# Performance work log

Measured on AMD Instinct MI355X. Metric: run time of the kernel, lower is better.

The kernel has to match this reference:

```python
import jax, jax.numpy as jnp
import numpy as np

B, T, IN_DIM, N_UNITS, OUT_DIM = 512, 64, 21, 128, 1
D = IN_DIM - 2  # 19 features fed to FF_attention_module
NPP_IDX, POPU_IDX = 0, 16
INIT_STD = 0.02


def setup_inputs() -> dict:
    key = jax.random.key(0)
    ks = jax.random.split(key, 21)
    init = lambda k, shape: jax.random.normal(k, shape, jnp.float32) * INIT_STD
    n = N_UNITS
    return {
        "x": jax.random.normal(ks[0], (B, T, IN_DIM), jnp.float32),
        "U_j": init(ks[1], (D, 1, n)),
        "W_j": init(ks[2], (D, n, n)),
        "b_j": init(ks[3], (D, n)),
        "Wi_w": init(ks[4], (D * n, D * (n + 1))),
        "Wi_b": init(ks[5], (D * n,)),
        "Wf_w": init(ks[6], (D * n, D * (n + 1))),
        "Wf_b": init(ks[7], (D * n,)),
        "Wo_w": init(ks[8], (D * n, D * (n + 1))),
        "Wo_b": init(ks[9], (D * n,)),
        "F_alpha_n": init(ks[10], (D, n, 1)),
        "F_alpha_n_b": init(ks[11], (D, 1)),
        "Fbeta_w": init(ks[12], (1, 2 * n)),
        "Fbeta_b": init(ks[13], (1,)),
        "Phi_w": init(ks[14], (OUT_DIM, 2 * n)),
        "Phi_b": init(ks[15], (OUT_DIM,)),
        "fa_w": init(ks[16], (1, 1)),
        "fa_b": init(ks[17], (1,)),
        "hs_w": init(ks[18], (1, 1)),
        "hs_b": init(ks[19], (1,)),
    }


def reference(x, U_j, W_j, b_j, Wi_w, Wi_b, Wf_w, Wf_b, Wo_w, Wo_b,
              F_alpha_n, F_alpha_n_b, Fbeta_w, Fbeta_b, Phi_w, Phi_b,
              fa_w, fa_b, hs_w, hs_b):
    # --- feature slicing for the IMV-LSTM branch (variational dropout is eval-mode identity) ---
    x_FF = jnp.concatenate([x[:, :, :POPU_IDX], x[:, :, -3:]], axis=-1)  # [B,T,D]
    bsz = x.shape[0]

    def step(carry, x_t):
        h, c = carry  # h: [B,D,n], c: [B,D*n]
        # per-variable candidate: tanh(h @ W_j + x_t * U_j + b_j)
        j = jnp.tanh(jnp.einsum('bij,ijk->bik', h, W_j)
                     + x_t[:, :, None] * U_j[:, 0, :]
                     + b_j)  # [B,D,n]
        inp = jnp.concatenate([x_t, h.reshape(bsz, -1)], axis=1)  # [B, D*(n+1)]
        i = jax.nn.sigmoid(inp @ Wi_w.T + Wi_b)
        f = jax.nn.sigmoid(inp @ Wf_w.T + Wf_b)
        o = jax.nn.sigmoid(inp @ Wo_w.T + Wo_b)
        c = c * f + i * j.reshape(bsz, -1)
        h = (o * jnp.tanh(c)).reshape(bsz, D, N_UNITS)
        return (h, c), h

    h0 = jnp.zeros((bsz, D, N_UNITS), x.dtype)
    c0 = jnp.zeros((bsz, D * N_UNITS), x.dtype)
    (h_fin, _), outs = jax.lax.scan(step, (h0, c0), jnp.swapaxes(x_FF, 0, 1))
    outputs = jnp.transpose(outs, (1, 0, 2, 3))  # [B,T,D,n]

    # temporal attention (alphas) over T
    alphas = jnp.exp(jnp.tanh(jnp.einsum('btij,ijk->btik', outputs, F_alpha_n) + F_alpha_n_b))
    alphas = alphas / jnp.sum(alphas, axis=1, keepdims=True)  # [B,T,D,1]
    g_n = jnp.sum(alphas * outputs, axis=1)  # [B,D,n]

    hg = jnp.concatenate([g_n, h_fin], axis=2)  # [B,D,2n]
    mu = hg @ Phi_w.T + Phi_b  # [B,D,OUT_DIM]
    betas = jnp.exp(jnp.tanh(hg @ Fbeta_w.T + Fbeta_b))  # [B,D,1]
    betas = betas / jnp.sum(betas, axis=1, keepdims=True)
    mean = jnp.sum(betas * mu, axis=1)  # [B,OUT_DIM]
    f_FF = jax.nn.sigmoid(mean)

    # limitation gates on last timestep
    f_npp = jax.nn.sigmoid(x[:, -1, NPP_IDX:NPP_IDX + 1] @ fa_w.T + fa_b)
    f_popu = jax.nn.sigmoid(x[:, -1, POPU_IDX:POPU_IDX + 1] @ hs_w.T + hs_b)
    return f_FF * f_npp * f_popu
```

## Files before the change

### kernel.cpp

```cpp
#include <hip/hip_runtime.h>
#include <hip/hip_bf16.h>


#define B_SZ 512
#define T_SZ 64
#define IN_DIMX 21
#define D_F 19
#define G_SZ 2432
#define NPAIR 9728
#define NK16 154
#define HFRAGS 152

typedef __attribute__((ext_vector_type(8))) short bf16x8;
typedef __attribute__((ext_vector_type(16))) float f32x16;

__device__ __forceinline__ float sigmoidf_(float v) { return 1.0f / (1.0f + expf(-v)); }
__device__ __forceinline__ int fmap(int j) { return j < 16 ? j : j + 2; }

__device__ __forceinline__ size_t hidx(int b, int gg) {
    int mb2 = b >> 6, r = b & 63, mi = r >> 5, bl = r & 31;
    int k16 = gg >> 4, half = (gg >> 3) & 1, e = gg & 7;
    return ((((size_t)(mb2 * 2 + mi) * HFRAGS + k16) * 64) + bl + 32 * half) * 8 + e;
}

__global__ __launch_bounds__(256) void prep_kernel(
    const float* __restrict__ x,
    const float* __restrict__ Wi, const float* __restrict__ Wf, const float* __restrict__ Wo,
    const float* __restrict__ Wj,
    __hip_bfloat16* __restrict__ Wt2,
    __hip_bfloat16* __restrict__ Wjt2,
    __hip_bfloat16* __restrict__ xfr,
    __hip_bfloat16* __restrict__ hfr0,
    float* __restrict__ apre)
{
    int i = blockIdx.x * 256 + threadIdx.x;
    const int NWT = 3 * 19 * 4 * NK16 * 512;
    if (i < NWT) {
        int e = i & 7, lane = (i >> 3) & 63, fi = i >> 9;
        int k16 = fi % NK16, ff = fi / NK16;
        int s = ff & 3, ff2 = ff >> 2;
        int d = ff2 % 19, gate = ff2 / 19;
        int gcol = d * 128 + s * 32 + (lane & 31);
        int k = k16 * 16 + (lane >> 5) * 8 + e;
        const float* W = gate == 0 ? Wi : (gate == 1 ? Wf : Wo);
        float v = 0.0f;
        if (k < 2432)      v = W[gcol * 2451 + 19 + k];
        else if (k < 2451) v = W[gcol * 2451 + (k - 2432)];
        Wt2[i] = __float2bfloat16(v);
        return;
    }
    i -= NWT;
    if (i < 19 * 4 * 8 * 512) {
        int e = i & 7, lane = (i >> 3) & 63, fi = i >> 9;
        int k16 = fi & 7, ff = fi >> 3;
        int s = ff & 3, d = ff >> 2;
        int col = s * 32 + (lane & 31);
        int kin = k16 * 16 + (lane >> 5) * 8 + e;
        Wjt2[i] = __float2bfloat16(Wj[d * 16384 + kin * 128 + col]);
        return;
    }
    i -= 19 * 4 * 8 * 512;
    if (i < 64 * 8 * 2 * 2 * 512) {
        int e = i & 7, lane = (i >> 3) & 63, fi = i >> 9;
        int k16 = fi & 1, ff = fi >> 1;
        int mi = ff & 1, ff2 = ff >> 1;
        int mb = ff2 & 7, tt = ff2 >> 3;
        int b = mb * 64 + mi * 32 + (lane & 31);
        int kloc = k16 * 16 + (lane >> 5) * 8 + e;
        float v = 0.0f;
        if (kloc < 19) v = x[(b * T_SZ + tt) * IN_DIMX + fmap(kloc)];
        xfr[i] = __float2bfloat16(v);
        return;
    }
    i -= 64 * 8 * 2 * 2 * 512;
    if (i < 8 * 2 * HFRAGS * 512) { hfr0[i] = __float2bfloat16(0.0f); return; }
    i -= 8 * 2 * HFRAGS * 512;
    if (i < 2 * NPAIR) apre[i] = 0.0f;
}

#define LOADSET(aa0, aa1, b00, b01, b10, b11, b20, b21, kk) do { \
    int f_ = 2 * (kk); \
    if ((kk) == 76) { aa0 = pAx[0]; aa1 = pAx[64]; } \
    else { aa0 = pA[(size_t)f_ * 64]; aa1 = pA[(size_t)f_ * 64 + 64]; } \
    b00 = pB0[(size_t)f_ * 64]; b01 = pB0[(size_t)f_ * 64 + 64]; \
    b10 = pB1[(size_t)f_ * 64]; b11 = pB1[(size_t)f_ * 64 + 64]; \
    b20 = pB2[(size_t)f_ * 64]; b21 = pB2[(size_t)f_ * 64 + 64]; } while (0)

#define MFMASET(aa0, aa1, b00, b01, b10, b11, b20, b21) do { \
    acc0 = __builtin_amdgcn_mfma_f32_32x32x16_bf16(aa0, b00, acc0, 0, 0, 0); \
    acc1 = __builtin_amdgcn_mfma_f32_32x32x16_bf16(aa0, b10, acc1, 0, 0, 0); \
    acc2 = __builtin_amdgcn_mfma_f32_32x32x16_bf16(aa0, b20, acc2, 0, 0, 0); \
    acc0 = __builtin_amdgcn_mfma_f32_32x32x16_bf16(aa1, b01, acc0, 0, 0, 0); \
    acc1 = __builtin_amdgcn_mfma_f32_32x32x16_bf16(aa1, b11, acc1, 0, 0, 0); \
    acc2 = __builtin_amdgcn_mfma_f32_32x32x16_bf16(aa1, b21, acc2, 0, 0, 0); } while (0)

__global__ __launch_bounds__(512, 2) void step_kernel(
    int t,
    const __hip_bfloat16* __restrict__ Wt2,
    const __hip_bfloat16* __restrict__ Wjt2,
    const __hip_bfloat16* __restrict__ xfr,
    const __hip_bfloat16* __restrict__ hcur,
    __hip_bfloat16* __restrict__ hnext,
    float* __restrict__ cbuf,
    float* __restrict__ apre,
    float* __restrict__ asum,
    float* __restrict__ gacc,
    const float* __restrict__ x,
    const float* __restrict__ Uj, const float* __restrict__ bj,
    const float* __restrict__ Wib, const float* __restrict__ Wfb, const float* __restrict__ Wob,
    const float* __restrict__ Fa, const float* __restrict__ Fab)
{
    __shared__ __align__(16) __hip_bfloat16 strans[8][1024];
    const int tid = threadIdx.x;
    const int g = 19 * (blockIdx.x & 7) + (blockIdx.x >> 3);
    const int nb = g >> 3, mb = g & 7;
    const int w = tid >> 6, lane = tid & 63;
    const int mi = w >> 2, s = w & 3;

    const bf16x8* pA  = (const bf16x8*)hcur + ((size_t)(mb * 2 + mi) * HFRAGS) * 64 + lane;
    const bf16x8* pAx = (const bf16x8*)xfr + ((size_t)((t * 8 + mb) * 2 + mi) * 2) * 64 + lane;
    const bf16x8* pB0 = (const bf16x8*)Wt2 + ((size_t)(0 * 76 + nb * 4 + s) * NK16) * 64 + lane;
    const bf16x8* pB1 = (const bf16x8*)Wt2 + ((size_t)(1 * 76 + nb * 4 + s) * NK16) * 64 + lane;
    const bf16x8* pB2 = (const bf16x8*)Wt2 + ((size_t)(2 * 76 + nb * 4 + s) * NK16) * 64 + lane;

    f32x16 acc0 = (f32x16)0.0f, acc1 = (f32x16)0.0f, acc2 = (f32x16)0.0f;
    bf16x8 aE0, aE1, bE00, bE01, bE10, bE11, bE20, bE21;
    bf16x8 aO0, aO1, bO00, bO01, bO10, bO11, bO20, bO21;

    LOADSET(aE0, aE1, bE00, bE01, bE10, bE11, bE20, bE21, 0);
    for (int kk2 = 0; kk2 < 39; ++kk2) {
        if (kk2 < 38) LOADSET(aO0, aO1, bO00, bO01, bO10, bO11, bO20, bO21, 2 * kk2 + 1);
        MFMASET(aE0, aE1, bE00, bE01, bE10, bE11, bE20, bE21);
        if (kk2 < 38) {
            LOADSET(aE0, aE1, bE00, bE01, bE10, bE11, bE20, bE21, 2 * kk2 + 2);
            MFMASET(aO0, aO1, bO00, bO01, bO10, bO11, bO20, bO21);
        }
    }

    if (t > 0) {
        int tp1 = (t - 1) & 1;
        int quarter = tid >> 7, k = tid & 127;
        for (int it = 0; it < 16; ++it) {
            int pair = g * 64 + it * 4 + quarter;
            int d = pair % 19, b = pair / 19;
            float a = expf(tanhf(apre[tp1 * NPAIR + pair] + Fab[d]));
            int idx = b * G_SZ + d * 128 + k;
            float hvv = __bfloat162float(hcur[hidx(b, d * 128 + k)]);
            if (t == 1) gacc[idx] = a * hvv; else gacc[idx] += a * hvv;
            if (k == 0) {
                if (t == 1) asum[pair] = a; else asum[pair] += a;
                apre[tp1 * NPAIR + pair] = 0.0f;
            }
        }
    }

    f32x16 aj = (f32x16)0.0f;
    const bf16x8* pAj = (const bf16x8*)hcur + ((size_t)(mb * 2 + mi) * HFRAGS + nb * 8) * 64 + lane;
    const bf16x8* pBj = (const bf16x8*)Wjt2 + ((size_t)(nb * 4 + s) * 8) * 64 + lane;
#pragma unroll
    for (int k16 = 0; k16 < 8; ++k16)
        aj = __builtin_amdgcn_mfma_f32_32x32x16_bf16(pAj[k16 * 64], pBj[k16 * 64], aj, 0, 0, 0);

    const int colg = nb * 128 + s * 32 + (lane & 31);
    const int kw = colg & 127;
    const float wib = Wib[colg], wfb = Wfb[colg], wob = Wob[colg];
    const float uj = Uj[nb * 128 + kw], bjv = bj[nb * 128 + kw], fav = Fa[nb * 128 + kw];
    const int xcol = fmap(nb);
    const int rbase = mb * 64 + mi * 32;

#pragma unroll
    for (int q = 0; q < 16; ++q) {
        int r = (q & 3) + 8 * (q >> 2) + 4 * (lane >> 5);
        int b = rbase + r;
        float iv = sigmoidf_(acc0[q] + wib);
        float fv = sigmoidf_(acc1[q] + wfb);
        float ov = sigmoidf_(acc2[q] + wob);
        float xv = x[(b * T_SZ + t) * IN_DIMX + xcol];
        float jv = tanhf(aj[q] + xv * uj + bjv);
        float cold = (t > 0) ? cbuf[(size_t)b * G_SZ + colg] : 0.0f;
        float cv = cold * fv + iv * jv;
        cbuf[(size_t)b * G_SZ + colg] = cv;
        float hv = ov * tanhf(cv);
        strans[w][r * 32 + (lane & 31)] = __float2bfloat16(hv);
        float psum = hv * fav;
#pragma unroll
        for (int m2 = 1; m2 < 32; m2 <<= 1) psum += __shfl_xor(psum, m2, 64);
        if ((lane & 31) == 0) atomicAdd(&apre[(t & 1) * NPAIR + b * 19 + nb], psum);
    }
#pragma unroll
    for (int hh = 0; hh < 2; ++hh) {
        bf16x8 hv8 = *(const bf16x8*)&strans[w][(lane & 31) * 32 + hh * 16 + (lane >> 5) * 8];
        size_t frag = (size_t)(mb * 2 + mi) * HFRAGS + nb * 8 + s * 2 + hh;
        *((bf16x8*)hnext + frag * 64 + lane) = hv8;
    }
}

__global__ __launch_bounds__(256) void final_kernel(
    const float* __restrict__ x,
    const __hip_bfloat16* __restrict__ h63,
    const float* __restrict__ apre, float* __restrict__ asum, float* __restrict__ gacc,
    const float* __restrict__ Fab,
    const float* __restrict__ Fbw, const float* __restrict__ Fbb,
    const float* __restrict__ Pw,  const float* __restrict__ Pb,
    const float* __restrict__ faw, const float* __restrict__ fab,
    const float* __restrict__ hsw, const float* __restrict__ hsb,
    float* __restrict__ out)
{
    const int b = blockIdx.x, tid = threadIdx.x;
    for (int e = tid; e < G_SZ; e += 256) {
        int d = e >> 7;
        float a = expf(tanhf(apre[NPAIR + b * 19 + d] + Fab[d]));
        gacc[b * G_SZ + e] += a * __bfloat162float(h63[hidx(b, e)]);
    }
    if (tid < 19) asum[b * 19 + tid] += expf(tanhf(apre[NPAIR + b * 19 + tid] + Fab[tid]));
    __syncthreads();

    const int wv = tid >> 6, lane = tid & 63;
    __shared__ float snum[4], sden[4];
    float num = 0.0f, den = 0.0f;
    for (int d = wv; d < 19; d += 4) {
        float asv = asum[b * 19 + d];
        float mua = 0.0f, bea = 0.0f;
#pragma unroll
        for (int j2 = 0; j2 < 4; ++j2) {
            int e = lane + j2 * 64;
            float hg = (e < 128) ? (gacc[b * G_SZ + d * 128 + e] / asv)
                                 : __bfloat162float(h63[hidx(b, d * 128 + (e - 128))]);
            mua += hg * Pw[e];
            bea += hg * Fbw[e];
        }
        for (int m = 1; m < 64; m <<= 1) { mua += __shfl_xor(mua, m, 64); bea += __shfl_xor(bea, m, 64); }
        if (lane == 0) {
            float mu = mua + Pb[0];
            float be = expf(tanhf(bea + Fbb[0]));
            num += be * mu; den += be;
        }
    }
    if (lane == 0) { snum[wv] = num; sden[wv] = den; }
    __syncthreads();
    if (tid == 0) {
        float n = 0.0f, dd = 0.0f;
        for (int w2 = 0; w2 < 4; ++w2) { n += snum[w2]; dd += sden[w2]; }
        float fFF = sigmoidf_(n / dd);
        float xn = x[(b * T_SZ + 63) * IN_DIMX + 0];
        float xp = x[(b * T_SZ + 63) * IN_DIMX + 16];
        float fn = sigmoidf_(xn * faw[0] + fab[0]);
        float fp = sigmoidf_(xp * hsw[0] + hsb[0]);
        out[b] = fFF * fn * fp;
    }
}

extern "C" void kernel_launch(void* const* d_in, const int* in_sizes, int n_in,
                              void* d_out, int out_size, void* d_ws, size_t ws_size,
                              hipStream_t stream) {
    const float* x   = (const float*)d_in[0];
    const float* Uj  = (const float*)d_in[1];
    const float* Wj  = (const float*)d_in[2];
    const float* bj  = (const float*)d_in[3];
    const float* Wi  = (const float*)d_in[4];
    const float* Wib = (const float*)d_in[5];
    const float* Wf  = (const float*)d_in[6];
    const float* Wfb = (const float*)d_in[7];
    const float* Wo  = (const float*)d_in[8];
    const float* Wob = (const float*)d_in[9];
    const float* Fa  = (const float*)d_in[10];
    const float* Fab = (const float*)d_in[11];
    const float* Fbw = (const float*)d_in[12];
    const float* Fbb = (const float*)d_in[13];
    const float* Pw  = (const float*)d_in[14];
    const float* Pb  = (const float*)d_in[15];
    const float* faw = (const float*)d_in[16];
    const float* fab = (const float*)d_in[17];
    const float* hsw = (const float*)d_in[18];
    const float* hsb = (const float*)d_in[19];

    char* ws = (char*)d_ws;
    size_t off = 0;
    auto alloc = [&](size_t bytes) { void* p = ws + off; off += (bytes + 255) & ~(size_t)255; return p; };

    __hip_bfloat16* Wt2  = (__hip_bfloat16*)alloc((size_t)3 * 19 * 4 * NK16 * 512 * 2);
    __hip_bfloat16* Wjt2 = (__hip_bfloat16*)alloc((size_t)19 * 4 * 8 * 512 * 2);
    __hip_bfloat16* xfr  = (__hip_bfloat16*)alloc((size_t)64 * 8 * 2 * 2 * 512 * 2);
    __hip_bfloat16* hfr  = (__hip_bfloat16*)alloc((size_t)2 * 8 * 2 * HFRAGS * 512 * 2);
    float* cbuf  = (float*)alloc((size_t)B_SZ * G_SZ * 4);
    float* apre  = (float*)alloc((size_t)2 * NPAIR * 4);
    float* asumb = (float*)alloc((size_t)NPAIR * 4);
    float* gacc  = (float*)alloc((size_t)B_SZ * G_SZ * 4);

    const size_t PREP_TOTAL = (size_t)3 * 19 * 4 * NK16 * 512 + 19 * 4 * 8 * 512
                            + (size_t)64 * 8 * 2 * 2 * 512 + (size_t)8 * 2 * HFRAGS * 512 + 2 * NPAIR;
    prep_kernel<<<(int)((PREP_TOTAL + 255) / 256), 256, 0, stream>>>(
        x, Wi, Wf, Wo, Wj, Wt2, Wjt2, xfr, hfr, apre);

    const size_t HB = (size_t)8 * 2 * HFRAGS * 512;
    for (int t = 0; t < T_SZ; ++t) {
        step_kernel<<<152, 512, 0, stream>>>(t, Wt2, Wjt2, xfr,
            hfr + (t & 1) * HB, hfr + ((t + 1) & 1) * HB,
            cbuf, apre, asumb, gacc,
            x, Uj, bj, Wib, Wfb, Wob, Fa, Fab);
    }
    final_kernel<<<B_SZ, 256, 0, stream>>>(x, hfr , apre, asumb, gacc,
        Fab, Fbw, Fbb, Pw, Pb, faw, fab, hsw, hsb, (float*)d_out);
}
```

Baseline: 5.111 ms.

## Fuse per-timestep launches into persistent kernel with grid barrier and register state

Result: no change. 5.019 ms (-1.8%).

```diff
diff --git a/kernel.cpp b/kernel.cpp
--- a/kernel.cpp
+++ b/kernel.cpp
@@ -10,6 +10,7 @@
 #define NPAIR 9728
 #define NK16 154
 #define HFRAGS 152
+#define NBLK 152
 
 typedef __attribute__((ext_vector_type(8))) short bf16x8;
 typedef __attribute__((ext_vector_type(16))) float f32x16;
@@ -31,7 +32,7 @@
     __hip_bfloat16* __restrict__ Wjt2,
     __hip_bfloat16* __restrict__ xfr,
     __hip_bfloat16* __restrict__ hfr0,
-    float* __restrict__ apre)
+    int* __restrict__ sync)
 {
     int i = blockIdx.x * 256 + threadIdx.x;
     const int NWT = 3 * 19 * 4 * NK16 * 512;
@@ -75,8 +76,10 @@
     i -= 64 * 8 * 2 * 2 * 512;
     if (i < 8 * 2 * HFRAGS * 512) { hfr0[i] = __float2bfloat16(0.0f); return; }
     i -= 8 * 2 * HFRAGS * 512;
-    if (i < 2 * NPAIR) apre[i] = 0.0f;
-}
+    if (i < 64) sync[i] = 0;
+}
+
+#define SBAR __builtin_amdgcn_sched_barrier(0)
 
 #define LOADSET(aa0, aa1, b00, b01, b10, b11, b20, b21, kk) do { \
     int f_ = 2 * (kk); \
@@ -94,112 +97,148 @@
     acc1 = __builtin_amdgcn_mfma_f32_32x32x16_bf16(aa1, b11, acc1, 0, 0, 0); \
     acc2 = __builtin_amdgcn_mfma_f32_32x32x16_bf16(aa1, b21, acc2, 0, 0, 0); } while (0)
 
-__global__ __launch_bounds__(512, 2) void step_kernel(
-    int t,
+__global__ __launch_bounds__(512, 2) void step_persist(
     const __hip_bfloat16* __restrict__ Wt2,
     const __hip_bfloat16* __restrict__ Wjt2,
     const __hip_bfloat16* __restrict__ xfr,
-    const __hip_bfloat16* __restrict__ hcur,
-    __hip_bfloat16* __restrict__ hnext,
-    float* __restrict__ cbuf,
-    float* __restrict__ apre,
-    float* __restrict__ asum,
-    float* __restrict__ gacc,
+    __hip_bfloat16* __restrict__ hfr,
+    float* __restrict__ gaccG,
+    float* __restrict__ asumG,
+    int* __restrict__ sync,
     const float* __restrict__ x,
     const float* __restrict__ Uj, const float* __restrict__ bj,
     const float* __restrict__ Wib, const float* __restrict__ Wfb, const float* __restrict__ Wob,
     const float* __restrict__ Fa, const float* __restrict__ Fab)
 {
     __shared__ __align__(16) __hip_bfloat16 strans[8][1024];
+    __shared__ float a_lds[64];
     const int tid = threadIdx.x;
-    const int g = 19 * (blockIdx.x & 7) + (blockIdx.x >> 3);
-    const int nb = g >> 3, mb = g & 7;
+    const int bid = blockIdx.x;
+
+    int nb, mb;
+    if (bid < 128) { int xc = bid & 7, j = bid >> 3; nb = (j >> 3) * 8 + xc; mb = j & 7; }
+    else           { int r2 = bid - 128; nb = 16 + (r2 >> 3); mb = r2 & 7; }
+
     const int w = tid >> 6, lane = tid & 63;
     const int mi = w >> 2, s = w & 3;
-
-    const bf16x8* pA  = (const bf16x8*)hcur + ((size_t)(mb * 2 + mi) * HFRAGS) * 64 + lane;
-    const bf16x8* pAx = (const bf16x8*)xfr + ((size_t)((t * 8 + mb) * 2 + mi) * 2) * 64 + lane;
-    const bf16x8* pB0 = (const bf16x8*)Wt2 + ((size_t)(0 * 76 + nb * 4 + s) * NK16) * 64 + lane;
-    const bf16x8* pB1 = (const bf16x8*)Wt2 + ((size_t)(1 * 76 + nb * 4 + s) * NK16) * 64 + lane;
-    const bf16x8* pB2 = (const bf16x8*)Wt2 + ((size_t)(2 * 76 + nb * 4 + s) * NK16) * 64 + lane;
-
-    f32x16 acc0 = (f32x16)0.0f, acc1 = (f32x16)0.0f, acc2 = (f32x16)0.0f;
-    bf16x8 aE0, aE1, bE00, bE01, bE10, bE11, bE20, bE21;
-    bf16x8 aO0, aO1, bO00, bO01, bO10, bO11, bO20, bO21;
-
-    LOADSET(aE0, aE1, bE00, bE01, bE10, bE11, bE20, bE21, 0);
-    for (int kk2 = 0; kk2 < 39; ++kk2) {
-        if (kk2 < 38) LOADSET(aO0, aO1, bO00, bO01, bO10, bO11, bO20, bO21, 2 * kk2 + 1);
-        MFMASET(aE0, aE1, bE00, bE01, bE10, bE11, bE20, bE21);
-        if (kk2 < 38) {
-            LOADSET(aE0, aE1, bE00, bE01, bE10, bE11, bE20, bE21, 2 * kk2 + 2);
-            MFMASET(aO0, aO1, bO00, bO01, bO10, bO11, bO20, bO21);
-        }
-    }
-
-    if (t > 0) {
-        int tp1 = (t - 1) & 1;
-        int quarter = tid >> 7, k = tid & 127;
-        for (int it = 0; it < 16; ++it) {
-            int pair = g * 64 + it * 4 + quarter;
-            int d = pair % 19, b = pair / 19;
-            float a = expf(tanhf(apre[tp1 * NPAIR + pair] + Fab[d]));
-            int idx = b * G_SZ + d * 128 + k;
-            float hvv = __bfloat162float(hcur[hidx(b, d * 128 + k)]);
-            if (t == 1) gacc[idx] = a * hvv; else gacc[idx] += a * hvv;
-            if (k == 0) {
-                if (t == 1) asum[pair] = a; else asum[pair] += a;
-                apre[tp1 * NPAIR + pair] = 0.0f;
-            }
-        }
-    }
-
-    f32x16 aj = (f32x16)0.0f;
-    const bf16x8* pAj = (const bf16x8*)hcur + ((size_t)(mb * 2 + mi) * HFRAGS + nb * 8) * 64 + lane;
-    const bf16x8* pBj = (const bf16x8*)Wjt2 + ((size_t)(nb * 4 + s) * 8) * 64 + lane;
-#pragma unroll
-    for (int k16 = 0; k16 < 8; ++k16)
-        aj = __builtin_amdgcn_mfma_f32_32x32x16_bf16(pAj[k16 * 64], pBj[k16 * 64], aj, 0, 0, 0);
+    const int rl = lane & 15; (void)rl;
 
     const int colg = nb * 128 + s * 32 + (lane & 31);
     const int kw = colg & 127;
     const float wib = Wib[colg], wfb = Wfb[colg], wob = Wob[colg];
     const float uj = Uj[nb * 128 + kw], bjv = bj[nb * 128 + kw], fav = Fa[nb * 128 + kw];
+    const float fab_s = Fab[nb];
     const int xcol = fmap(nb);
     const int rbase = mb * 64 + mi * 32;
+    const size_t HB = (size_t)8 * 2 * HFRAGS * 512;
+
+    float cc[16], gaccr[16];
+#pragma unroll
+    for (int q = 0; q < 16; ++q) { cc[q] = 0.0f; gaccr[q] = 0.0f; }
+    float asum_r = 0.0f;
+
+    if (w == 0) a_lds[lane] = 0.0f;
+    __syncthreads();
+
+    const bf16x8* pB0 = (const bf16x8*)Wt2 + ((size_t)(0 * 76 + nb * 4 + s) * NK16) * 64 + lane;
+    const bf16x8* pB1 = (const bf16x8*)Wt2 + ((size_t)(1 * 76 + nb * 4 + s) * NK16) * 64 + lane;
+    const bf16x8* pB2 = (const bf16x8*)Wt2 + ((size_t)(2 * 76 + nb * 4 + s) * NK16) * 64 + lane;
+    const bf16x8* pBj = (const bf16x8*)Wjt2 + ((size_t)(nb * 4 + s) * 8) * 64 + lane;
+
+#pragma unroll 1
+    for (int t = 0; t < T_SZ; ++t) {
+        const __hip_bfloat16* hcur = hfr + (t & 1) * HB;
+        __hip_bfloat16* hnext = hfr + ((t + 1) & 1) * HB;
+
+        const bf16x8* pA  = (const bf16x8*)hcur + ((size_t)(mb * 2 + mi) * HFRAGS) * 64 + lane;
+        const bf16x8* pAx = (const bf16x8*)xfr + ((size_t)((t * 8 + mb) * 2 + mi) * 2) * 64 + lane;
+
+        f32x16 acc0 = (f32x16)0.0f, acc1 = (f32x16)0.0f, acc2 = (f32x16)0.0f;
+        bf16x8 aE0, aE1, bE00, bE01, bE10, bE11, bE20, bE21;
+        bf16x8 aO0, aO1, bO00, bO01, bO10, bO11, bO20, bO21;
+
+        LOADSET(aE0, aE1, bE00, bE01, bE10, bE11, bE20, bE21, 0);
+        for (int kk2 = 0; kk2 < 39; ++kk2) {
+            if (kk2 < 38) { SBAR; LOADSET(aO0, aO1, bO00, bO01, bO10, bO11, bO20, bO21, 2 * kk2 + 1); SBAR; }
+            MFMASET(aE0, aE1, bE00, bE01, bE10, bE11, bE20, bE21);
+            if (kk2 < 38) {
+                SBAR; LOADSET(aE0, aE1, bE00, bE01, bE10, bE11, bE20, bE21, 2 * kk2 + 2); SBAR;
+                MFMASET(aO0, aO1, bO00, bO01, bO10, bO11, bO20, bO21);
+            }
+        }
+
+        f32x16 aj = (f32x16)0.0f;
+        const bf16x8* pAj = (const bf16x8*)hcur + ((size_t)(mb * 2 + mi) * HFRAGS + nb * 8) * 64 + lane;
+#pragma unroll
+        for (int k16 = 0; k16 < 8; ++k16)
+            aj = __builtin_amdgcn_mfma_f32_32x32x16_bf16(pAj[k16 * 64], pBj[k16 * 64], aj, 0, 0, 0);
+
+#pragma unroll
+        for (int q = 0; q < 16; ++q) {
+            int r = (q & 3) + 8 * (q >> 2) + 4 * (lane >> 5);
+            int b = rbase + r;
+            float iv = sigmoidf_(acc0[q] + wib);
+            float fv = sigmoidf_(acc1[q] + wfb);
+            float ov = sigmoidf_(acc2[q] + wob);
+            float xv = x[(b * T_SZ + t) * IN_DIMX + xcol];
+            float jv = tanhf(aj[q] + xv * uj + bjv);
+            float cv = cc[q] * fv + iv * jv;
+            cc[q] = cv;
+            float hv = ov * tanhf(cv);
+            strans[w][r * 32 + (lane & 31)] = __float2bfloat16(hv);
+            float psum = hv * fav;
+#pragma unroll
+            for (int m2 = 1; m2 < 32; m2 <<= 1) psum += __shfl_xor(psum, m2, 64);
+            if ((lane & 31) == 0) atomicAdd(&a_lds[mi * 32 + r], psum);
+        }
+#pragma unroll
+        for (int hh = 0; hh < 2; ++hh) {
+            bf16x8 hv8 = *(const bf16x8*)&strans[w][(lane & 31) * 32 + hh * 16 + (lane >> 5) * 8];
+            size_t frag = (size_t)(mb * 2 + mi) * HFRAGS + nb * 8 + s * 2 + hh;
+            *((bf16x8*)hnext + frag * 64 + lane) = hv8;
+        }
+
+        __syncthreads();
+        if (w == 0) {
+            float av = expf(tanhf(a_lds[lane] + fab_s));
+            a_lds[lane] = av;
+            asum_r += av;
+        }
+        __syncthreads();
+#pragma unroll
+        for (int q = 0; q < 16; ++q) {
+            int r = (q & 3) + 8 * (q >> 2) + 4 * (lane >> 5);
+            gaccr[q] += a_lds[mi * 32 + r] * __bfloat162float(strans[w][r * 32 + (lane & 31)]);
+        }
+        __syncthreads();
+        if (w == 0) a_lds[lane] = 0.0f;
+
+        __syncthreads();
+        if (tid == 0) {
+            __threadfence();
+            int v = atomicAdd(&sync[0], 1);
+            if (v == NBLK * (t + 1) - 1) {
+                atomicExch(&sync[1], t + 1);
+            } else {
+                while (atomicAdd(&sync[1], 0) < t + 1) __builtin_amdgcn_s_sleep(8);
+            }
+            __threadfence();
+        }
+        __syncthreads();
+    }
 
 #pragma unroll
     for (int q = 0; q < 16; ++q) {
         int r = (q & 3) + 8 * (q >> 2) + 4 * (lane >> 5);
-        int b = rbase + r;
-        float iv = sigmoidf_(acc0[q] + wib);
-        float fv = sigmoidf_(acc1[q] + wfb);
-        float ov = sigmoidf_(acc2[q] + wob);
-        float xv = x[(b * T_SZ + t) * IN_DIMX + xcol];
-        float jv = tanhf(aj[q] + xv * uj + bjv);
-        float cold = (t > 0) ? cbuf[(size_t)b * G_SZ + colg] : 0.0f;
-        float cv = cold * fv + iv * jv;
-        cbuf[(size_t)b * G_SZ + colg] = cv;
-        float hv = ov * tanhf(cv);
-        strans[w][r * 32 + (lane & 31)] = __float2bfloat16(hv);
-        float psum = hv * fav;
-#pragma unroll
-        for (int m2 = 1; m2 < 32; m2 <<= 1) psum += __shfl_xor(psum, m2, 64);
-        if ((lane & 31) == 0) atomicAdd(&apre[(t & 1) * NPAIR + b * 19 + nb], psum);
-    }
-#pragma unroll
-    for (int hh = 0; hh < 2; ++hh) {
-        bf16x8 hv8 = *(const bf16x8*)&strans[w][(lane & 31) * 32 + hh * 16 + (lane >> 5) * 8];
-        size_t frag = (size_t)(mb * 2 + mi) * HFRAGS + nb * 8 + s * 2 + hh;
-        *((bf16x8*)hnext + frag * 64 + lane) = hv8;
-    }
+        gaccG[(size_t)(rbase + r) * G_SZ + colg] = gaccr[q];
+    }
+    if (w == 0) asumG[(mb * 64 + lane) * 19 + nb] = asum_r;
 }
 
 __global__ __launch_bounds__(256) void final_kernel(
     const float* __restrict__ x,
     const __hip_bfloat16* __restrict__ h63,
-    const float* __restrict__ apre, float* __restrict__ asum, float* __restrict__ gacc,
-    const float* __restrict__ Fab,
+    const float* __restrict__ asum, const float* __restrict__ gacc,
     const float* __restrict__ Fbw, const float* __restrict__ Fbb,
     const float* __restrict__ Pw,  const float* __restrict__ Pb,
     const float* __restrict__ faw, const float* __restrict__ fab,
@@ -207,14 +246,6 @@
     float* __restrict__ out)
 {
     const int b = blockIdx.x, tid = threadIdx.x;
-    for (int e = tid; e < G_SZ; e += 256) {
-        int d = e >> 7;
-        float a = expf(tanhf(apre[NPAIR + b * 19 + d] + Fab[d]));
-        gacc[b * G_SZ + e] += a * __bfloat162float(h63[hidx(b, e)]);
-    }
-    if (tid < 19) asum[b * 19 + tid] += expf(tanhf(apre[NPAIR + b * 19 + tid] + Fab[tid]));
-    __syncthreads();
-
     const int wv = tid >> 6, lane = tid & 63;
     __shared__ float snum[4], sden[4];
     float num = 0.0f, den = 0.0f;
@@ -282,23 +313,18 @@
     __hip_bfloat16* Wjt2 = (__hip_bfloat16*)alloc((size_t)19 * 4 * 8 * 512 * 2);
     __hip_bfloat16* xfr  = (__hip_bfloat16*)alloc((size_t)64 * 8 * 2 * 2 * 512 * 2);
     __hip_bfloat16* hfr  = (__hip_bfloat16*)alloc((size_t)2 * 8 * 2 * HFRAGS * 512 * 2);
-    float* cbuf  = (float*)alloc((size_t)B_SZ * G_SZ * 4);
-    float* apre  = (float*)alloc((size_t)2 * NPAIR * 4);
+    float* gacc  = (float*)alloc((size_t)B_SZ * G_SZ * 4);
     float* asumb = (float*)alloc((size_t)NPAIR * 4);
-    float* gacc  = (float*)alloc((size_t)B_SZ * G_SZ * 4);
+    int*   syncb = (int*)alloc(64 * 4);
 
     const size_t PREP_TOTAL = (size_t)3 * 19 * 4 * NK16 * 512 + 19 * 4 * 8 * 512
-                            + (size_t)64 * 8 * 2 * 2 * 512 + (size_t)8 * 2 * HFRAGS * 512 + 2 * NPAIR;
+                            + (size_t)64 * 8 * 2 * 2 * 512 + (size_t)8 * 2 * HFRAGS * 512 + 64;
     prep_kernel<<<(int)((PREP_TOTAL + 255) / 256), 256, 0, stream>>>(
-        x, Wi, Wf, Wo, Wj, Wt2, Wjt2, xfr, hfr, apre);
-
-    const size_t HB = (size_t)8 * 2 * HFRAGS * 512;
-    for (int t = 0; t < T_SZ; ++t) {
-        step_kernel<<<152, 512, 0, stream>>>(t, Wt2, Wjt2, xfr,
-            hfr + (t & 1) * HB, hfr + ((t + 1) & 1) * HB,
-            cbuf, apre, asumb, gacc,
-            x, Uj, bj, Wib, Wfb, Wob, Fa, Fab);
-    }
-    final_kernel<<<B_SZ, 256, 0, stream>>>(x, hfr , apre, asumb, gacc,
-        Fab, Fbw, Fbb, Pw, Pb, faw, fab, hsw, hsb, (float*)d_out);
-}
+        x, Wi, Wf, Wo, Wj, Wt2, Wjt2, xfr, hfr, syncb);
+
+    step_persist<<<NBLK, 512, 0, stream>>>(Wt2, Wjt2, xfr, hfr, gacc, asumb, syncb,
+        x, Uj, bj, Wib, Wfb, Wob, Fa, Fab);
+
+    final_kernel<<<B_SZ, 256, 0, stream>>>(x, hfr , asumb, gacc,
+        Fbw, Fbb, Pw, Pb, faw, fab, hsw, hsb, (float*)d_out);
+}
```
